# Performance work log

Measured on AMD Instinct MI355X. Metric: run time of the kernel, lower is better.

The kernel has to match this reference:

```python
import jax, jax.numpy as jnp
import numpy as np

N_EMBED = 768
NUM_HEADS = 12
HEAD_SIZE = N_EMBED // NUM_HEADS
EPS = 1e-6


def layer_norm(x, gamma, beta):
    # torch .var() is unbiased (ddof=1)
    mean = x.mean(-1, keepdims=True)
    var = jnp.var(x, axis=-1, keepdims=True, ddof=1)
    xhat = (x - mean) / jnp.sqrt(var + EPS)
    return gamma * xhat + beta


def setup_inputs() -> dict:
    key = jax.random.key(0)
    ks = jax.random.split(key, 10)
    B, S, D = 4, 2048, N_EMBED
    H = 4 * D
    s = 0.02
    return {
        "x": jax.random.normal(ks[0], (B, S, D), jnp.float32),
        "wq": jax.random.normal(ks[1], (D, D), jnp.float32) * s,
        "wk": jax.random.normal(ks[2], (D, D), jnp.float32) * s,
        "wv": jax.random.normal(ks[3], (D, D), jnp.float32) * s,
        "wo": jax.random.normal(ks[4], (D, D), jnp.float32) * s,
        "w1": jax.random.normal(ks[5], (D, H), jnp.float32) * s,
        "b1": jnp.zeros((H,), jnp.float32),
        "w2": jax.random.normal(ks[6], (H, D), jnp.float32) * s,
        "b2": jnp.zeros((D,), jnp.float32),
        "gamma1": jnp.ones((D,), jnp.float32),
        "beta1": jnp.zeros((D,), jnp.float32),
        "gamma2": jnp.ones((D,), jnp.float32),
        "beta2": jnp.zeros((D,), jnp.float32),
    }


def reference(x, wq, wk, wv, wo, w1, b1, w2, b2, gamma1, beta1, gamma2, beta2):
    B, S, D = x.shape
    Hh, hs = NUM_HEADS, HEAD_SIZE

    # --- pre-LN causal self-attention ---
    xn = layer_norm(x, gamma1, beta1)
    q = (xn @ wq).reshape(B, S, Hh, hs).transpose(0, 2, 1, 3)  # [B,H,S,hs]
    k = (xn @ wk).reshape(B, S, Hh, hs).transpose(0, 2, 1, 3)
    v = (xn @ wv).reshape(B, S, Hh, hs).transpose(0, 2, 1, 3)

    scale = 1.0 / np.sqrt(hs).astype(np.float32)
    scores = jnp.einsum("bhqd,bhkd->bhqk", q, k) * scale  # [B,H,S,S]
    causal = jnp.tril(jnp.ones((S, S), bool))
    scores = jnp.where(causal, scores, -jnp.inf)
    weights = jax.nn.softmax(scores, axis=-1)
    attn = jnp.einsum("bhqk,bhkd->bhqd", weights, v)  # [B,H,S,hs]
    attn = attn.transpose(0, 2, 1, 3).reshape(B, S, D)
    x = x + attn @ wo

    # --- pre-LN MLP ---
    xn = layer_norm(x, gamma2, beta2)
    h = jax.nn.relu(xn @ w1 + b1)
    x = x + (h @ w2 + b2)
    return x
```

## Files before the change

### kernel.cpp

```cpp
#include <hip/hip_runtime.h>
#include <hip/hip_bf16.h>
#include <math.h>

#define BATCH 4
#define SEQ   2048
#define DMODEL 768
#define NHEAD 12
#define HS    64
#define HID   3072
#define NROWS (BATCH*SEQ)
#define QKVN  (3*DMODEL)
#define EPS   1e-6f

typedef __attribute__((ext_vector_type(8))) short bf16x8;
typedef __attribute__((ext_vector_type(4))) float f32x4;

__device__ inline ushort f2b(float f) {
    union { float f; unsigned u; } x; x.f = f;
    unsigned u = x.u;
    unsigned r = (u + 0x7FFFu + ((u >> 16) & 1u)) >> 16;
    return (ushort)r;
}

#define GLDS16(g, l) __builtin_amdgcn_global_load_lds( \
    (const __attribute__((address_space(1))) void*)(g), \
    (__attribute__((address_space(3))) void*)(l), 16, 0, 0)

__global__ __launch_bounds__(256) void convert_w4(const float* __restrict__ p0,
                                                  const float* __restrict__ p1,
                                                  const float* __restrict__ p2,
                                                  const float* __restrict__ p3,
                                                  ushort* __restrict__ out) {
    const float* srcs[4] = { p0, p1, p2, p3 };
    const float* in = srcs[blockIdx.z];
    ushort* dst = out + (size_t)blockIdx.z * DMODEL * DMODEL;
    __shared__ float tile[32][33];
    const int bx = blockIdx.x * 32;
    const int by = blockIdx.y * 32;
    const int tx = threadIdx.x & 31, ty = threadIdx.x >> 5;
    #pragma unroll
    for (int i = 0; i < 32; i += 8)
        tile[ty + i][tx] = in[(size_t)(by + ty + i) * DMODEL + bx + tx];
    __syncthreads();
    #pragma unroll
    for (int i = 0; i < 32; i += 8)
        dst[(size_t)(bx + ty + i) * DMODEL + by + tx] = f2b(tile[tx][ty + i]);
}

__global__ __launch_bounds__(256) void convert_w(const float* __restrict__ in,
                                                 ushort* __restrict__ out,
                                                 int K, int N) {
    __shared__ float tile[32][33];
    const int bx = blockIdx.x * 32;
    const int by = blockIdx.y * 32;
    const int tx = threadIdx.x & 31, ty = threadIdx.x >> 5;
    #pragma unroll
    for (int i = 0; i < 32; i += 8)
        tile[ty + i][tx] = in[(size_t)(by + ty + i) * N + bx + tx];
    __syncthreads();
    #pragma unroll
    for (int i = 0; i < 32; i += 8)
        out[(size_t)(bx + ty + i) * K + by + tx] = f2b(tile[tx][ty + i]);
}

__global__ __launch_bounds__(256) void transpose_v(const ushort* __restrict__ v,
                                                   ushort* __restrict__ vt) {
    const int st = blockIdx.x;
    const int bh = blockIdx.y;
    const int b = bh / NHEAD, h = bh % NHEAD;
    const ushort* src = v + ((size_t)b * SEQ) * QKVN + h * HS;
    ushort* dst = vt + ((size_t)bh * HS) * SEQ;
    __shared__ ushort t[64][65];
    const int col = threadIdx.x & 63;
    const int r0  = (threadIdx.x >> 6) * 16;
    #pragma unroll
    for (int i = 0; i < 16; ++i)
        t[col][r0 + i] = src[(size_t)(st * 64 + r0 + i) * QKVN + col];
    __syncthreads();
    #pragma unroll
    for (int i = 0; i < 16; ++i)
        dst[(size_t)(r0 + i) * SEQ + st * 64 + col] = t[r0 + i][col];
}

__global__ __launch_bounds__(256) void ln_kernel(const float* __restrict__ x,
                                                 const float* __restrict__ gamma,
                                                 const float* __restrict__ beta,
                                                 ushort* __restrict__ out) {
    const int row = blockIdx.x;
    const float* xr = x + (size_t)row * DMODEL;
    float s = 0.f, s2 = 0.f;
    for (int i = threadIdx.x; i < DMODEL; i += 256) {
        float v = xr[i];
        s += v; s2 += v * v;
    }
    for (int off = 32; off > 0; off >>= 1) {
        s  += __shfl_down(s,  off, 64);
        s2 += __shfl_down(s2, off, 64);
    }
    __shared__ float shs[4], shs2[4];
    int wid = threadIdx.x >> 6, lane = threadIdx.x & 63;
    if (lane == 0) { shs[wid] = s; shs2[wid] = s2; }
    __syncthreads();
    __shared__ float smean, srstd;
    if (threadIdx.x == 0) {
        float S  = shs[0] + shs[1] + shs[2] + shs[3];
        float S2 = shs2[0] + shs2[1] + shs2[2] + shs2[3];
        float mean = S / DMODEL;
        float var  = (S2 - DMODEL * mean * mean) / (DMODEL - 1);
        smean = mean;
        srstd = rsqrtf(var + EPS);
    }
    __syncthreads();
    float mean = smean, rstd = srstd;
    ushort* orow = out + (size_t)row * DMODEL;
    for (int i = threadIdx.x; i < DMODEL; i += 256) {
        orow[i] = f2b(gamma[i] * (xr[i] - mean) * rstd + beta[i]);
    }
}

#define GN 128
#define GK 64
#define GM 64
__global__ __launch_bounds__(256, 3) void gemm_mfma(const ushort* __restrict__ A,
                                                    const ushort* __restrict__ Bt,
                                                    const float* __restrict__ bias,
                                                    const float* __restrict__ res,
                                                    float* __restrict__ C,
                                                    ushort* __restrict__ Cb,
                                                    int M, int N, int K, int do_relu,
                                                    int scale_q) {
    __shared__ ushort As[2][GM * GK];
    __shared__ ushort Bs[2][GN * GK];
    const int tid  = threadIdx.x;
    const int lane = tid & 63, wave = tid >> 6;
    const int l16  = lane & 15, quad = lane >> 4;
    const int wr = wave >> 1, wc = wave & 1;

    const int nwg = gridDim.x * gridDim.y;
    int id = blockIdx.y * gridDim.x + blockIdx.x;
    if ((nwg & 7) == 0) {
        const int chunk = nwg >> 3;
        id = (id & 7) * chunk + (id >> 3);
    }
    const int bx = id % gridDim.x;
    const int by = id / gridDim.x;
    const int row0 = by * GM, col0 = bx * GN;

    f32x4 acc[2][4];
    #pragma unroll
    for (int i = 0; i < 2; ++i)
        #pragma unroll
        for (int j = 0; j < 4; ++j) acc[i][j] = (f32x4){0.f, 0.f, 0.f, 0.f};

    const ushort* Asrc[2];
    const ushort* Bsrc[4];
    #pragma unroll
    for (int i = 0; i < 2; ++i) {
        int c = tid + i * 256, m = c >> 3, j = c & 7;
        Asrc[i] = A + (size_t)(row0 + m) * K + (j ^ (m & 7)) * 8;
    }
    #pragma unroll
    for (int i = 0; i < 4; ++i) {
        int c = tid + i * 256, m = c >> 3, j = c & 7;
        Bsrc[i] = Bt + (size_t)(col0 + m) * K + (j ^ (m & 7)) * 8;
    }

    const int nk = K / GK;
    #pragma unroll
    for (int i = 0; i < 2; ++i) GLDS16(Asrc[i], &As[0][(tid + i * 256) * 8]);
    #pragma unroll
    for (int i = 0; i < 4; ++i)  GLDS16(Bsrc[i], &Bs[0][(tid + i * 256) * 8]);

    for (int kt = 0; kt < nk; ++kt) {
        const int p = kt & 1;
        __syncthreads();
        if (kt + 1 < nk) {
            const int k1 = (kt + 1) * GK;
            #pragma unroll
            for (int i = 0; i < 2; ++i) GLDS16(Asrc[i] + k1, &As[p ^ 1][(tid + i * 256) * 8]);
            #pragma unroll
            for (int i = 0; i < 4; ++i)  GLDS16(Bsrc[i] + k1, &Bs[p ^ 1][(tid + i * 256) * 8]);
        }

        #pragma unroll
        for (int s = 0; s < 2; ++s) {
            bf16x8 af[2], bfr[4];
            #pragma unroll
            for (int i = 0; i < 2; ++i) {
                int m = wr * 32 + i * 16 + l16;
                af[i] = *(const bf16x8*)&As[p][(m * 8 + (((s << 2) | quad) ^ (m & 7))) * 8];
            }
            #pragma unroll
            for (int j = 0; j < 4; ++j) {
                int n = wc * 64 + j * 16 + l16;
                bfr[j] = *(const bf16x8*)&Bs[p][(n * 8 + (((s << 2) | quad) ^ (n & 7))) * 8];
            }
            #pragma unroll
            for (int i = 0; i < 2; ++i)
                #pragma unroll
                for (int j = 0; j < 4; ++j)
                    acc[i][j] = __builtin_amdgcn_mfma_f32_16x16x32_bf16(af[i], bfr[j], acc[i][j], 0, 0, 0);
        }
    }

    #pragma unroll
    for (int i = 0; i < 2; ++i) {
        #pragma unroll
        for (int r = 0; r < 4; ++r) {
            int row = row0 + wr * 32 + i * 16 + quad * 4 + r;
            #pragma unroll
            for (int j = 0; j < 4; ++j) {
                int col = col0 + wc * 64 + j * 16 + l16;
                float v = acc[i][j][r];
                if (bias) v += bias[col];
                if (do_relu) v = fmaxf(v, 0.f);
                if (scale_q && col < DMODEL) v *= 0.125f;
                if (res) v += res[(size_t)row * N + col];
                if (Cb) Cb[(size_t)row * N + col] = f2b(v);
                else    C [(size_t)row * N + col] = v;
            }
        }
    }
}

#define HM 128
#define HN 128
#define HK 32
__global__ __launch_bounds__(256, 3) void gemm_big(const ushort* __restrict__ A,
                                                   const ushort* __restrict__ Bt,
                                                   const float* __restrict__ bias,
                                                   const float* __restrict__ res,
                                                   float* __restrict__ C,
                                                   ushort* __restrict__ Cb,
                                                   int M, int N, int K, int do_relu,
                                                   int scale_q) {
    __shared__ ushort As[3][HM * HK];
    __shared__ ushort Bs[3][HN * HK];
    const int tid  = threadIdx.x;
    const int lane = tid & 63, wave = tid >> 6;
    const int l16  = lane & 15, quad = lane >> 4;
    const int wr = wave >> 1, wc = wave & 1;

    const int nwg = gridDim.x * gridDim.y;
    int id = blockIdx.y * gridDim.x + blockIdx.x;
    if ((nwg & 7) == 0) {
        const int chunk = nwg >> 3;
        id = (id & 7) * chunk + (id >> 3);
    }
    const int bx = id % gridDim.x;
    const int by = id / gridDim.x;
    const int row0 = by * HM, col0 = bx * HN;

    f32x4 acc[4][4];
    #pragma unroll
    for (int i = 0; i < 4; ++i)
        #pragma unroll
        for (int j = 0; j < 4; ++j) acc[i][j] = (f32x4){0.f, 0.f, 0.f, 0.f};

    const ushort* Asrc[2];
    const ushort* Bsrc[2];
    #pragma unroll
    for (int i = 0; i < 2; ++i) {
        int c = tid + i * 256;
        int lr = c >> 3, pp = (c & 7) ^ (lr & 7);
        int m = lr * 2 + (pp >> 2), j = pp & 3;
        Asrc[i] = A  + (size_t)(row0 + m) * K + j * 8;
        Bsrc[i] = Bt + (size_t)(col0 + m) * K + j * 8;
    }

    const int nk = K / HK;

#define STAGE_BIG(kt, b) do { \
    const int _k = (kt) * HK; \
    GLDS16(Asrc[0] + _k, &As[b][tid * 8]); \
    GLDS16(Asrc[1] + _k, &As[b][(tid + 256) * 8]); \
    GLDS16(Bsrc[0] + _k, &Bs[b][tid * 8]); \
    GLDS16(Bsrc[1] + _k, &Bs[b][(tid + 256) * 8]); \
} while (0)

    STAGE_BIG(0, 0);
    STAGE_BIG(1, 1);

    int pc = 0, pn = 1, ps = 2;
    for (int t = 0; t < nk; ++t) {
        if (t + 1 < nk) asm volatile("s_waitcnt vmcnt(4)" ::: "memory");
        else            asm volatile("s_waitcnt vmcnt(0)" ::: "memory");
        __builtin_amdgcn_s_barrier();
        if (t + 2 < nk) STAGE_BIG(t + 2, ps);

        bf16x8 af[4], bfr[4];
        #pragma unroll
        for (int i = 0; i < 4; ++i) {
            int m = wr * 64 + i * 16 + l16;
            int ch = (m >> 1) * 8 + ((((m & 1) << 2) | quad) ^ ((m >> 1) & 7));
            af[i] = *(const bf16x8*)&As[pc][ch * 8];
        }
        #pragma unroll
        for (int j = 0; j < 4; ++j) {
            int n = wc * 64 + j * 16 + l16;
            int ch = (n >> 1) * 8 + ((((n & 1) << 2) | quad) ^ ((n >> 1) & 7));
            bfr[j] = *(const bf16x8*)&Bs[pc][ch * 8];
        }
        #pragma unroll
        for (int i = 0; i < 4; ++i)
            #pragma unroll
            for (int j = 0; j < 4; ++j)
                acc[i][j] = __builtin_amdgcn_mfma_f32_16x16x32_bf16(af[i], bfr[j], acc[i][j], 0, 0, 0);

        int tmp = pc; pc = pn; pn = ps; ps = tmp;
    }

    #pragma unroll
    for (int i = 0; i < 4; ++i) {
        #pragma unroll
        for (int r = 0; r < 4; ++r) {
            int row = row0 + wr * 64 + i * 16 + quad * 4 + r;
            #pragma unroll
            for (int j = 0; j < 4; ++j) {
                int col = col0 + wc * 64 + j * 16 + l16;
                float v = acc[i][j][r];
                if (bias) v += bias[col];
                if (do_relu) v = fmaxf(v, 0.f);
                if (scale_q && col < DMODEL) v *= 0.125f;
                if (res) v += res[(size_t)row * N + col];
                if (Cb) Cb[(size_t)row * N + col] = f2b(v);
                else    C [(size_t)row * N + col] = v;
            }
        }
    }
}

#define TQ 64
#define TK 64
#define PPAD 72
#define NQT (SEQ / TQ)

__global__ __launch_bounds__(256, 3) void fattn_kernel(const ushort* __restrict__ q,
                                                       const ushort* __restrict__ k,
                                                       const ushort* __restrict__ vt,
                                                       ushort* __restrict__ o,
                                                       int ldqkv) {
    const int pair = blockIdx.x;
    const int qts[2] = { pair, NQT - 1 - pair };
    const int bh = blockIdx.y;
    const int b = bh / NHEAD, h = bh % NHEAD;
    const int tid  = threadIdx.x;
    const int wave = tid >> 6;
    const int lane = tid & 63;
    const int l16  = lane & 15;
    const int quad = lane >> 4;

    __shared__ ushort Ks[2][TK * 64];
    __shared__ ushort Vs[2][HS * 64];
    __shared__ ushort Ps[4][16][PPAD];

    const size_t base  = ((size_t)b * SEQ) * ldqkv + (size_t)h * HS;
    const size_t baseO = ((size_t)b * SEQ) * DMODEL + (size_t)h * HS;
    const ushort* vth = vt + ((size_t)bh * HS) * SEQ;

    const int r0 = tid >> 3, j0 = (tid & 7) ^ (r0 & 7);
    const int r1 = (tid + 256) >> 3, j1 = (tid & 7) ^ (r1 & 7);
    const ushort* Ksrc0 = k + base + (size_t)r0 * ldqkv + j0 * 8;
    const ushort* Ksrc1 = k + base + (size_t)r1 * ldqkv + j1 * 8;
    const ushort* Vsrc0 = vth + (size_t)r0 * SEQ + j0 * 8;
    const ushort* Vsrc1 = vth + (size_t)r1 * SEQ + j1 * 8;

    bf16x8 qf[2][2];
    #pragma unroll
    for (int t = 0; t < 2; ++t) {
        int qrow = qts[t] * TQ + wave * 16 + l16;
        const ushort* qp = q + base + (size_t)qrow * ldqkv + quad * 8;
        qf[t][0] = *(const bf16x8*)(qp);
        qf[t][1] = *(const bf16x8*)(qp + 32);
    }

    f32x4 Oacc[2][4];
    float lrow[2][4];
    #pragma unroll
    for (int t = 0; t < 2; ++t) {
        #pragma unroll
        for (int f = 0; f < 4; ++f) Oacc[t][f] = (f32x4){0.f, 0.f, 0.f, 0.f};
        #pragma unroll
        for (int r = 0; r < 4; ++r) lrow[t][r] = 0.f;
    }

    const int ktiles = qts[1] + 1;
    GLDS16(Ksrc0, &Ks[0][tid * 8]);
    GLDS16(Ksrc1, &Ks[0][(tid + 256) * 8]);
    GLDS16(Vsrc0, &Vs[0][tid * 8]);
    GLDS16(Vsrc1, &Vs[0][(tid + 256) * 8]);

    for (int kt = 0; kt < ktiles; ++kt) {
        const int p = kt & 1;
        __syncthreads();
        if (kt + 1 < ktiles) {
            const size_t ko = (size_t)(kt + 1) * TK;
            GLDS16(Ksrc0 + ko * ldqkv, &Ks[p ^ 1][tid * 8]);
            GLDS16(Ksrc1 + ko * ldqkv, &Ks[p ^ 1][(tid + 256) * 8]);
            GLDS16(Vsrc0 + ko,         &Vs[p ^ 1][tid * 8]);
            GLDS16(Vsrc1 + ko,         &Vs[p ^ 1][(tid + 256) * 8]);
        }

        bf16x8 kb[4][2], vb[4][2];
        #pragma unroll
        for (int f = 0; f < 4; ++f) {
            int row = f * 16 + l16;
            kb[f][0] = *(const bf16x8*)&Ks[p][(row * 8 + (quad ^ (row & 7))) * 8];
            kb[f][1] = *(const bf16x8*)&Ks[p][(row * 8 + ((4 | quad) ^ (row & 7))) * 8];
            vb[f][0] = *(const bf16x8*)&Vs[p][(row * 8 + (quad ^ (row & 7))) * 8];
            vb[f][1] = *(const bf16x8*)&Vs[p][(row * 8 + ((4 | quad) ^ (row & 7))) * 8];
        }

        #pragma unroll
        for (int t = 0; t < 2; ++t) {
            const int qt = qts[t];
            if (kt > qt) continue;

            f32x4 S[4];
            #pragma unroll
            for (int f = 0; f < 4; ++f) {
                f32x4 a = (f32x4){0.f, 0.f, 0.f, 0.f};
                a = __builtin_amdgcn_mfma_f32_16x16x32_bf16(qf[t][0], kb[f][0], a, 0, 0, 0);
                a = __builtin_amdgcn_mfma_f32_16x16x32_bf16(qf[t][1], kb[f][1], a, 0, 0, 0);
                S[f] = a;
            }

            const int qrow_base = qt * TQ + wave * 16 + quad * 4;
            if (kt == qt) {
                #pragma unroll
                for (int f = 0; f < 4; ++f) {
                    int key = kt * TK + f * 16 + l16;
                    #pragma unroll
                    for (int r = 0; r < 4; ++r)
                        if (key > qrow_base + r) S[f][r] = -INFINITY;
                }
            }

            #pragma unroll
            for (int f = 0; f < 4; ++f) {
                #pragma unroll
                for (int r = 0; r < 4; ++r) {
                    float pv = __expf(S[f][r]);
                    S[f][r] = pv;
                    lrow[t][r] += pv;
                }
            }

            #pragma unroll
            for (int f = 0; f < 4; ++f)
                #pragma unroll
                for (int r = 0; r < 4; ++r)
                    Ps[wave][quad * 4 + r][f * 16 + l16] = f2b(S[f][r]);

            bf16x8 pa0 = *(const bf16x8*)&Ps[wave][l16][quad * 8];
            bf16x8 pa1 = *(const bf16x8*)&Ps[wave][l16][32 + quad * 8];
            #pragma unroll
            for (int f = 0; f < 4; ++f) {
                Oacc[t][f] = __builtin_amdgcn_mfma_f32_16x16x32_bf16(pa0, vb[f][0], Oacc[t][f], 0, 0, 0);
                Oacc[t][f] = __builtin_amdgcn_mfma_f32_16x16x32_bf16(pa1, vb[f][1], Oacc[t][f], 0, 0, 0);
            }
        }
    }

    #pragma unroll
    for (int t = 0; t < 2; ++t) {
        const int qrow = qts[t] * TQ + wave * 16 + quad * 4;
        #pragma unroll
        for (int r = 0; r < 4; ++r) {
            float l = lrow[t][r];
            #pragma unroll
            for (int m = 1; m < 16; m <<= 1) l += __shfl_xor(l, m, 64);
            float invl = 1.f / l;
            #pragma unroll
            for (int f = 0; f < 4; ++f)
                o[baseO + (size_t)(qrow + r) * DMODEL + f * 16 + l16] = f2b(Oacc[t][f][r] * invl);
        }
    }
}

extern "C" void kernel_launch(void* const* d_in, const int* in_sizes, int n_in,
                              void* d_out, int out_size, void* d_ws, size_t ws_size,
                              hipStream_t stream) {
    const float* x      = (const float*)d_in[0];
    const float* wq     = (const float*)d_in[1];
    const float* wk     = (const float*)d_in[2];
    const float* wv     = (const float*)d_in[3];
    const float* wo     = (const float*)d_in[4];
    const float* w1     = (const float*)d_in[5];
    const float* b1     = (const float*)d_in[6];
    const float* w2     = (const float*)d_in[7];
    const float* b2     = (const float*)d_in[8];
    const float* gamma1 = (const float*)d_in[9];
    const float* beta1  = (const float*)d_in[10];
    const float* gamma2 = (const float*)d_in[11];
    const float* beta2  = (const float*)d_in[12];
    float* out = (float*)d_out;

    char* ws = (char*)d_ws;
    ushort* buf_xn   = (ushort*)ws;
    ushort* buf_attn = buf_xn;
    ushort* buf_qkv  = (ushort*)(ws + 12582912);
    ushort* buf_h    = buf_qkv;
    ushort* w_qkv    = (ushort*)(ws + 12582912 + 50331648);
    ushort* w_ot     = w_qkv + (size_t)QKVN * DMODEL;
    ushort* w_1t     = w_ot + (size_t)DMODEL * DMODEL;
    ushort* w_2t     = w_1t + (size_t)HID * DMODEL;
    ushort* buf_vt   = (ushort*)d_out;

    convert_w4<<<dim3(DMODEL/32, DMODEL/32, 4), 256, 0, stream>>>(wq, wk, wv, wo, w_qkv);
    convert_w<<<dim3(HID/32,    DMODEL/32), 256, 0, stream>>>(w1, w_1t, DMODEL, HID);
    convert_w<<<dim3(DMODEL/32, HID/32),    256, 0, stream>>>(w2, w_2t, HID, DMODEL);

    ln_kernel<<<NROWS, 256, 0, stream>>>(x, gamma1, beta1, buf_xn);
    gemm_big<<<dim3(QKVN/HN, NROWS/HM), 256, 0, stream>>>(buf_xn, w_qkv, nullptr, nullptr,
                                                          nullptr, buf_qkv, NROWS, QKVN, DMODEL, 0, 1);
    transpose_v<<<dim3(SEQ/64, BATCH*NHEAD), 256, 0, stream>>>(buf_qkv + 2*DMODEL, buf_vt);
    fattn_kernel<<<dim3(NQT/2, BATCH*NHEAD), 256, 0, stream>>>(buf_qkv, buf_qkv + DMODEL,
                                                               buf_vt, buf_attn, QKVN);
    gemm_mfma<<<dim3(DMODEL/GN, NROWS/GM), 256, 0, stream>>>(buf_attn, w_ot, nullptr, x,
                                                             out, nullptr, NROWS, DMODEL, DMODEL, 0, 0);
    ln_kernel<<<NROWS, 256, 0, stream>>>(out, gamma2, beta2, buf_xn);
    gemm_big<<<dim3(HID/HN, NROWS/HM), 256, 0, stream>>>(buf_xn, w_1t, b1, nullptr,
                                                         nullptr, buf_h, NROWS, HID, DMODEL, 1, 0);
    gemm_mfma<<<dim3(DMODEL/GN, NROWS/GM), 256, 0, stream>>>(buf_h, w_2t, b2, out,
                                                             out, nullptr, NROWS, DMODEL, HID, 0, 0);
}
```

Measured before the change: 419.8 us.

## Triple-buffer small GEMM with K=32 stages and enlarge big GEMM to 256x128 tiles

The smaller output-projection and MLP-down GEMM moves from a double-buffered K=64 loop with __syncthreads to a triple-buffered K=32 pipeline. It uses manual vmcnt waits and the same paired-row swizzle already used by the big GEMM, so global loads overlap compute more deeply and more blocks fit per CU. The QKV and MLP-up GEMM is reworked to 512 threads with 256x128 tiles, which doubles A-tile reuse of each B tile and halves the grid. Risks are more register pressure from the raised launch-bounds occupancy targets, fewer blocks for the big GEMM, and an extra barrier per step from the smaller K tile.

```diff
diff --git a/kernel.cpp b/kernel.cpp
--- a/kernel.cpp
+++ b/kernel.cpp
@@ -119,9 +119,9 @@
 }
 
 #define GN 128
-#define GK 64
+#define GK 32
 #define GM 64
-__global__ __launch_bounds__(256, 3) void gemm_mfma(const ushort* __restrict__ A,
+__global__ __launch_bounds__(256, 4) void gemm_mfma(const ushort* __restrict__ A,
                                                     const ushort* __restrict__ Bt,
                                                     const float* __restrict__ bias,
                                                     const float* __restrict__ res,
@@ -129,8 +129,8 @@
                                                     ushort* __restrict__ Cb,
                                                     int M, int N, int K, int do_relu,
                                                     int scale_q) {
-    __shared__ ushort As[2][GM * GK];
-    __shared__ ushort Bs[2][GN * GK];
+    __shared__ ushort As[3][GM * GK];
+    __shared__ ushort Bs[3][GN * GK];
     const int tid  = threadIdx.x;
     const int lane = tid & 63, wave = tid >> 6;
     const int l16  = lane & 15, quad = lane >> 4;
@@ -152,55 +152,59 @@
         #pragma unroll
         for (int j = 0; j < 4; ++j) acc[i][j] = (f32x4){0.f, 0.f, 0.f, 0.f};
 
-    const ushort* Asrc[2];
-    const ushort* Bsrc[4];
+    const ushort* Asrc;
+    const ushort* Bsrc[2];
+    {
+        int c = tid, lr = c >> 3, pp = (c & 7) ^ (lr & 7);
+        int m = lr * 2 + (pp >> 2), j = pp & 3;
+        Asrc = A + (size_t)(row0 + m) * K + j * 8;
+    }
     #pragma unroll
     for (int i = 0; i < 2; ++i) {
-        int c = tid + i * 256, m = c >> 3, j = c & 7;
-        Asrc[i] = A + (size_t)(row0 + m) * K + (j ^ (m & 7)) * 8;
-    }
-    #pragma unroll
-    for (int i = 0; i < 4; ++i) {
-        int c = tid + i * 256, m = c >> 3, j = c & 7;
-        Bsrc[i] = Bt + (size_t)(col0 + m) * K + (j ^ (m & 7)) * 8;
+        int c = tid + i * 256, lr = c >> 3, pp = (c & 7) ^ (lr & 7);
+        int m = lr * 2 + (pp >> 2), j = pp & 3;
+        Bsrc[i] = Bt + (size_t)(col0 + m) * K + j * 8;
     }
 
     const int nk = K / GK;
-    #pragma unroll
-    for (int i = 0; i < 2; ++i) GLDS16(Asrc[i], &As[0][(tid + i * 256) * 8]);
-    #pragma unroll
-    for (int i = 0; i < 4; ++i)  GLDS16(Bsrc[i], &Bs[0][(tid + i * 256) * 8]);
-
-    for (int kt = 0; kt < nk; ++kt) {
-        const int p = kt & 1;
-        __syncthreads();
-        if (kt + 1 < nk) {
-            const int k1 = (kt + 1) * GK;
-            #pragma unroll
-            for (int i = 0; i < 2; ++i) GLDS16(Asrc[i] + k1, &As[p ^ 1][(tid + i * 256) * 8]);
-            #pragma unroll
-            for (int i = 0; i < 4; ++i)  GLDS16(Bsrc[i] + k1, &Bs[p ^ 1][(tid + i * 256) * 8]);
-        }
-
-        #pragma unroll
-        for (int s = 0; s < 2; ++s) {
-            bf16x8 af[2], bfr[4];
-            #pragma unroll
-            for (int i = 0; i < 2; ++i) {
-                int m = wr * 32 + i * 16 + l16;
-                af[i] = *(const bf16x8*)&As[p][(m * 8 + (((s << 2) | quad) ^ (m & 7))) * 8];
-            }
-            #pragma unroll
-            for (int j = 0; j < 4; ++j) {
-                int n = wc * 64 + j * 16 + l16;
-                bfr[j] = *(const bf16x8*)&Bs[p][(n * 8 + (((s << 2) | quad) ^ (n & 7))) * 8];
-            }
-            #pragma unroll
-            for (int i = 0; i < 2; ++i)
-                #pragma unroll
-                for (int j = 0; j < 4; ++j)
-                    acc[i][j] = __builtin_amdgcn_mfma_f32_16x16x32_bf16(af[i], bfr[j], acc[i][j], 0, 0, 0);
-        }
+
+#define STAGE_MF(kt, b) do { \
+    const int _k = (kt) * GK; \
+    GLDS16(Asrc + _k,    &As[b][tid * 8]); \
+    GLDS16(Bsrc[0] + _k, &Bs[b][tid * 8]); \
+    GLDS16(Bsrc[1] + _k, &Bs[b][(tid + 256) * 8]); \
+} while (0)
+
+    STAGE_MF(0, 0);
+    STAGE_MF(1, 1);
+
+    int pc = 0, pn = 1, ps = 2;
+    for (int t = 0; t < nk; ++t) {
+        if (t + 1 < nk) asm volatile("s_waitcnt vmcnt(3)" ::: "memory");
+        else            asm volatile("s_waitcnt vmcnt(0)" ::: "memory");
+        __builtin_amdgcn_s_barrier();
+        if (t + 2 < nk) STAGE_MF(t + 2, ps);
+
+        bf16x8 af[2], bfr[4];
+        #pragma unroll
+        for (int i = 0; i < 2; ++i) {
+            int m = wr * 32 + i * 16 + l16;
+            int ch = (m >> 1) * 8 + ((((m & 1) << 2) | quad) ^ ((m >> 1) & 7));
+            af[i] = *(const bf16x8*)&As[pc][ch * 8];
+        }
+        #pragma unroll
+        for (int j = 0; j < 4; ++j) {
+            int n = wc * 64 + j * 16 + l16;
+            int ch = (n >> 1) * 8 + ((((n & 1) << 2) | quad) ^ ((n >> 1) & 7));
+            bfr[j] = *(const bf16x8*)&Bs[pc][ch * 8];
+        }
+        #pragma unroll
+        for (int i = 0; i < 2; ++i)
+            #pragma unroll
+            for (int j = 0; j < 4; ++j)
+                acc[i][j] = __builtin_amdgcn_mfma_f32_16x16x32_bf16(af[i], bfr[j], acc[i][j], 0, 0, 0);
+
+        int tmp = pc; pc = pn; pn = ps; ps = tmp;
     }
 
     #pragma unroll
@@ -223,10 +227,10 @@
     }
 }
 
-#define HM 128
+#define HM 256
 #define HN 128
 #define HK 32
-__global__ __launch_bounds__(256, 3) void gemm_big(const ushort* __restrict__ A,
+__global__ __launch_bounds__(512, 4) void gemm_big(const ushort* __restrict__ A,
                                                    const ushort* __restrict__ Bt,
                                                    const float* __restrict__ bias,
                                                    const float* __restrict__ res,
@@ -239,7 +243,7 @@
     const int tid  = threadIdx.x;
     const int lane = tid & 63, wave = tid >> 6;
     const int l16  = lane & 15, quad = lane >> 4;
-    const int wr = wave >> 1, wc = wave & 1;
+    const int wr = wave & 3, wc = wave >> 2;
 
     const int nwg = gridDim.x * gridDim.y;
     int id = blockIdx.y * gridDim.x + blockIdx.x;
@@ -258,14 +262,17 @@
         for (int j = 0; j < 4; ++j) acc[i][j] = (f32x4){0.f, 0.f, 0.f, 0.f};
 
     const ushort* Asrc[2];
-    const ushort* Bsrc[2];
+    const ushort* Bsrc;
     #pragma unroll
     for (int i = 0; i < 2; ++i) {
-        int c = tid + i * 256;
-        int lr = c >> 3, pp = (c & 7) ^ (lr & 7);
+        int c = tid + i * 512, lr = c >> 3, pp = (c & 7) ^ (lr & 7);
         int m = lr * 2 + (pp >> 2), j = pp & 3;
-        Asrc[i] = A  + (size_t)(row0 + m) * K + j * 8;
-        Bsrc[i] = Bt + (size_t)(col0 + m) * K + j * 8;
+        Asrc[i] = A + (size_t)(row0 + m) * K + j * 8;
+    }
+    {
+        int c = tid, lr = c >> 3, pp = (c & 7) ^ (lr & 7);
+        int m = lr * 2 + (pp >> 2), j = pp & 3;
+        Bsrc = Bt + (size_t)(col0 + m) * K + j * 8;
     }
 
     const int nk = K / HK;
@@ -273,9 +280,8 @@
 #define STAGE_BIG(kt, b) do { \
     const int _k = (kt) * HK; \
     GLDS16(Asrc[0] + _k, &As[b][tid * 8]); \
-    GLDS16(Asrc[1] + _k, &As[b][(tid + 256) * 8]); \
-    GLDS16(Bsrc[0] + _k, &Bs[b][tid * 8]); \
-    GLDS16(Bsrc[1] + _k, &Bs[b][(tid + 256) * 8]); \
+    GLDS16(Asrc[1] + _k, &As[b][(tid + 512) * 8]); \
+    GLDS16(Bsrc + _k,    &Bs[b][tid * 8]); \
 } while (0)
 
     STAGE_BIG(0, 0);
@@ -283,7 +289,7 @@
 
     int pc = 0, pn = 1, ps = 2;
     for (int t = 0; t < nk; ++t) {
-        if (t + 1 < nk) asm volatile("s_waitcnt vmcnt(4)" ::: "memory");
+        if (t + 1 < nk) asm volatile("s_waitcnt vmcnt(3)" ::: "memory");
         else            asm volatile("s_waitcnt vmcnt(0)" ::: "memory");
         __builtin_amdgcn_s_barrier();
         if (t + 2 < nk) STAGE_BIG(t + 2, ps);
@@ -512,7 +518,7 @@
     convert_w<<<dim3(DMODEL/32, HID/32),    256, 0, stream>>>(w2, w_2t, HID, DMODEL);
 
     ln_kernel<<<NROWS, 256, 0, stream>>>(x, gamma1, beta1, buf_xn);
-    gemm_big<<<dim3(QKVN/HN, NROWS/HM), 256, 0, stream>>>(buf_xn, w_qkv, nullptr, nullptr,
+    gemm_big<<<dim3(QKVN/HN, NROWS/HM), 512, 0, stream>>>(buf_xn, w_qkv, nullptr, nullptr,
                                                           nullptr, buf_qkv, NROWS, QKVN, DMODEL, 0, 1);
     transpose_v<<<dim3(SEQ/64, BATCH*NHEAD), 256, 0, stream>>>(buf_qkv + 2*DMODEL, buf_vt);
     fattn_kernel<<<dim3(NQT/2, BATCH*NHEAD), 256, 0, stream>>>(buf_qkv, buf_qkv + DMODEL,
@@ -520,7 +526,7 @@
     gemm_mfma<<<dim3(DMODEL/GN, NROWS/GM), 256, 0, stream>>>(buf_attn, w_ot, nullptr, x,
                                                              out, nullptr, NROWS, DMODEL, DMODEL, 0, 0);
     ln_kernel<<<NROWS, 256, 0, stream>>>(out, gamma2, beta2, buf_xn);
-    gemm_big<<<dim3(HID/HN, NROWS/HM), 256, 0, stream>>>(buf_xn, w_1t, b1, nullptr,
+    gemm_big<<<dim3(HID/HN, NROWS/HM), 512, 0, stream>>>(buf_xn, w_1t, b1, nullptr,
                                                          nullptr, buf_h, NROWS, HID, DMODEL, 1, 0);
     gemm_mfma<<<dim3(DMODEL/GN, NROWS/GM), 256, 0, stream>>>(buf_h, w_2t, b2, out,
                                                              out, nullptr, NROWS, DMODEL, HID, 0, 0);
```

Measured after the change: 442.7 us. +5.4%, slower.
